# Kernel optimization log

Measured on AMD Instinct MI355X. Metric: run time of the kernel, lower is better.

## Reference

```python
import jax, jax.numpy as jnp
import numpy as np

NUM_RBF = 64
CUTOFF = 5.0
N_GRAPHS = 64


def _rbf_expand(d):
    # Gaussian RBF expansion on [0, CUTOFF] with cosine cutoff envelope.
    mus = jnp.linspace(0.0, CUTOFF, NUM_RBF, dtype=d.dtype)  # [M]
    gamma = (NUM_RBF / CUTOFF) ** 2  # 1 / spacing^2
    fc = 0.5 * (jnp.cos(jnp.pi * d / CUTOFF) + 1.0) * (d < CUTOFF)  # [E]
    return jnp.exp(-gamma * (d[:, None] - mus[None, :]) ** 2) * fc[:, None]  # [E,M]


def setup_inputs() -> dict:
    key = jax.random.key(0)
    k0, k1, k2, k3, k4, k5 = jax.random.split(key, 6)
    N, E, T = 50000, 1600000, 25
    pos = jax.random.normal(k0, (N, 3), jnp.float32) * 3.0
    edge_index = jax.random.randint(k1, (2, E), 0, N)
    atom_types = jax.random.randint(k2, (N,), 0, T)
    batch = jnp.sort(jax.random.randint(k3, (N,), 0, N_GRAPHS))
    rbf_params = jax.random.normal(k4, (T, T, NUM_RBF), jnp.float32)
    radial_filters = jax.random.uniform(k5, (T, T, NUM_RBF), jnp.float32)
    return {
        "pos": pos,
        "rbf_params": rbf_params,
        "radial_filters": radial_filters,
        "edge_index": edge_index,
        "atom_types": atom_types,
        "batch": batch,
    }


def reference(pos, rbf_params, radial_filters, edge_index, atom_types, batch):
    src, dst = edge_index[0], edge_index[1]
    # distances (no cell shifts)
    diff = pos[dst] - pos[src]                       # [E,3]
    d = jnp.sqrt(jnp.sum(diff * diff, axis=-1) + 1e-12)  # [E]
    # type-pair lookup with canonical ordering (sender <= receiver)
    s = atom_types[src]
    r = atom_types[dst]
    lo = jnp.minimum(s, r)
    hi = jnp.maximum(s, r)
    params = rbf_params[lo, hi]        # [E,M]
    filt = radial_filters[lo, hi]      # [E,M] (already in [0,1])
    expn = _rbf_expand(d) * filt       # filtered RBF expansion
    e_edge = jnp.sum(expn * params, axis=1)  # [E]
    # reduce per-edge energies to per-graph energies
    bmap = batch[src]
    energy = jax.ops.segment_sum(e_edge, bmap, num_segments=N_GRAPHS)  # [G]
    return energy
```

## Files before the change

kernel.cpp:

```cpp
#include <hip/hip_runtime.h>
#include <math.h>

#define NUM_RBF 64
#define N_GRAPHS 64


__global__ __launch_bounds__(256) void build_table_kernel(
    const float4* __restrict__ p, const float4* __restrict__ f,
    float4* __restrict__ C, int n4)
{
    int i = blockIdx.x * blockDim.x + threadIdx.x;
    if (i < n4) {
        float4 a = p[i], b = f[i];
        C[i] = make_float4(a.x * b.x, a.y * b.y, a.z * b.z, a.w * b.w);
    }
}

__global__ __launch_bounds__(256) void pack_nodes_kernel(
    const float* __restrict__ pos, const int* __restrict__ types,
    const int* __restrict__ batch, float4* __restrict__ rec, int N)
{
    int i = blockIdx.x * blockDim.x + threadIdx.x;
    if (i < N) {
        int bits = (types[i] & 0xFF) | ((batch[i] & 0xFF) << 8);
        rec[i] = make_float4(pos[3 * i], pos[3 * i + 1], pos[3 * i + 2],
                             __int_as_float(bits));
    }
}

#define CUTOFF_F      5.0f
#define GAMMA_F       163.84f
#define SPACING_F     (5.0f / 63.0f)
#define INV_SPACING_F (63.0f / 5.0f)
#define PI_OVER_C_F   (3.14159265358979f / 5.0f)

__device__ __forceinline__ void edge_body(
    float4 rs, float4 rd, const float4* __restrict__ C4, int T,
    float* __restrict__ bins)
{
    const float dx = rd.x - rs.x;
    const float dy = rd.y - rs.y;
    const float dz = rd.z - rs.z;
    const float d  = sqrtf(dx * dx + dy * dy + dz * dz + 1e-12f);
    if (d >= CUTOFF_F) return;

    const int sb = __float_as_int(rs.w);
    const int db = __float_as_int(rd.w);
    const int ts = sb & 0xFF;
    const int td = db & 0xFF;
    const int lo = min(ts, td);
    const int hi = max(ts, td);
    const int base = (lo * T + hi) * NUM_RBF;

    const float c = d * INV_SPACING_F;
    int a0 = ((int)floorf(c - 3.5f)) & ~3;
    a0 = max(0, min(NUM_RBF - 12, a0));

    const float4* w = C4 + ((base + a0) >> 2);
    float acc = 0.0f;
    float delta = d - (float)a0 * SPACING_F;
#pragma unroll
    for (int j = 0; j < 3; ++j) {
        const float4 cv = w[j];
        const float d0 = delta;
        const float d1 = delta - SPACING_F;
        const float d2 = delta - 2.0f * SPACING_F;
        const float d3 = delta - 3.0f * SPACING_F;
        acc += cv.x * __expf(-GAMMA_F * d0 * d0);
        acc += cv.y * __expf(-GAMMA_F * d1 * d1);
        acc += cv.z * __expf(-GAMMA_F * d2 * d2);
        acc += cv.w * __expf(-GAMMA_F * d3 * d3);
        delta -= 4.0f * SPACING_F;
    }
    const float fc = 0.5f * (__cosf(PI_OVER_C_F * d) + 1.0f);
    atomicAdd(&bins[(sb >> 8) & 0xFF], acc * fc);
}

__global__ __launch_bounds__(256) void edge_energy_kernel(
    const int*    __restrict__ edge_index,
    const float4* __restrict__ rec,
    const float4* __restrict__ C4,
    float*        __restrict__ partial,
    int E, int T)
{
    __shared__ float bins[N_GRAPHS];
    for (int i = threadIdx.x; i < N_GRAPHS; i += blockDim.x) bins[i] = 0.0f;
    __syncthreads();

    const int nfull  = E >> 2;
    const int stride = gridDim.x * blockDim.x;
    const int gid    = blockIdx.x * blockDim.x + threadIdx.x;

    for (int q = gid; q < nfull; q += stride) {
        const int e0 = q << 2;
        const int4 sv = *(const int4*)(edge_index + e0);
        const int4 tv = *(const int4*)(edge_index + E + e0);

        const float4 rs0 = rec[sv.x], rd0 = rec[tv.x];
        const float4 rs1 = rec[sv.y], rd1 = rec[tv.y];
        const float4 rs2 = rec[sv.z], rd2 = rec[tv.z];
        const float4 rs3 = rec[sv.w], rd3 = rec[tv.w];

        edge_body(rs0, rd0, C4, T, bins);
        edge_body(rs1, rd1, C4, T, bins);
        edge_body(rs2, rd2, C4, T, bins);
        edge_body(rs3, rd3, C4, T, bins);
    }

    if (gid == 0) {
        for (int e = nfull << 2; e < E; ++e) {
            const float4 rs = rec[edge_index[e]];
            const float4 rd = rec[edge_index[E + e]];
            edge_body(rs, rd, C4, T, bins);
        }
    }

    __syncthreads();
    for (int i = threadIdx.x; i < N_GRAPHS; i += blockDim.x)
        partial[blockIdx.x * N_GRAPHS + i] = bins[i];
}

__global__ __launch_bounds__(256) void reduce_kernel(
    const float* __restrict__ partial, float* __restrict__ out, int nblocks)
{
    const int g = blockIdx.x;
    float s = 0.0f;
    for (int i = threadIdx.x; i < nblocks; i += blockDim.x)
        s += partial[i * N_GRAPHS + g];

    for (int off = 32; off > 0; off >>= 1)
        s += __shfl_down(s, off, 64);

    __shared__ float red[4];
    const int wave = threadIdx.x >> 6;
    const int lane = threadIdx.x & 63;
    if (lane == 0) red[wave] = s;
    __syncthreads();
    if (threadIdx.x == 0)
        out[g] = red[0] + red[1] + red[2] + red[3];
}

extern "C" void kernel_launch(void* const* d_in, const int* in_sizes, int n_in,
                              void* d_out, int out_size, void* d_ws, size_t ws_size,
                              hipStream_t stream) {
    const float* pos            = (const float*)d_in[0];
    const float* rbf_params     = (const float*)d_in[1];
    const float* radial_filters = (const float*)d_in[2];
    const int*   edge_index     = (const int*)d_in[3];
    const int*   atom_types     = (const int*)d_in[4];
    const int*   batch          = (const int*)d_in[5];
    float*       out            = (float*)d_out;

    const int E = in_sizes[3] / 2;
    const int N = in_sizes[4];
    int T = 1;
    while ((T + 1) * (T + 1) * NUM_RBF <= in_sizes[1]) ++T;
    const int tbl_elems = T * T * NUM_RBF;

    float*  Ctab    = (float*)d_ws;
    float4* recs    = (float4*)((char*)d_ws + ((size_t)tbl_elems * 4 + 255) / 256 * 256);
    float*  partial = (float*)((char*)recs + (size_t)N * 16);

    const int nq = E >> 2;
    int nblocks = (nq + 255) / 256;
    const size_t part_off = (size_t)((char*)partial - (char*)d_ws);
    const size_t avail = (ws_size > part_off) ? (ws_size - part_off) : 0;
    const int maxb = (int)(avail / (N_GRAPHS * sizeof(float)));
    if (nblocks > maxb) nblocks = maxb > 0 ? maxb : 1;
    if (nblocks < 1) nblocks = 1;

    build_table_kernel<<<(tbl_elems / 4 + 255) / 256, 256, 0, stream>>>(
        (const float4*)rbf_params, (const float4*)radial_filters,
        (float4*)Ctab, tbl_elems / 4);
    pack_nodes_kernel<<<(N + 255) / 256, 256, 0, stream>>>(
        pos, atom_types, batch, recs, N);
    edge_energy_kernel<<<nblocks, 256, 0, stream>>>(
        edge_index, recs, (const float4*)Ctab, partial, E, T);
    reduce_kernel<<<N_GRAPHS, 256, 0, stream>>>(partial, out, nblocks);
}
```

Baseline: 97.57 us.

## Compute Gaussian RBF window via exp recurrence, fuse prologue kernels, nontemporal edge loads

Replaces the 12 per-edge exponentials with three exps plus a multiplicative recurrence. It expands the Gaussian around the centre bin, so each neighbour's term comes from the previous one times a ratio built from constant factors. The two setup kernels are merged into one launch, and edge-index loads now use nontemporal hints so streaming indices do not pollute cache. The recurrence adds rounding error, and u or ui may overflow or underflow for edges far from the centre bin.

```diff
diff --git a/kernel.cpp b/kernel.cpp
--- a/kernel.cpp
+++ b/kernel.cpp
@@ -4,38 +4,38 @@
 #define NUM_RBF 64
 #define N_GRAPHS 64
 
+typedef int   int4v   __attribute__((ext_vector_type(4)));
+typedef float float4v __attribute__((ext_vector_type(4)));
 
-__global__ __launch_bounds__(256) void build_table_kernel(
-    const float4* __restrict__ p, const float4* __restrict__ f,
-    float4* __restrict__ C, int n4)
+
+__global__ __launch_bounds__(256) void prologue_kernel(
+    const float4v* __restrict__ p, const float4v* __restrict__ f,
+    float4v* __restrict__ C, int n4,
+    const float* __restrict__ pos, const int* __restrict__ types,
+    const int* __restrict__ batch, float4v* __restrict__ rec, int N)
 {
     int i = blockIdx.x * blockDim.x + threadIdx.x;
-    if (i < n4) {
-        float4 a = p[i], b = f[i];
-        C[i] = make_float4(a.x * b.x, a.y * b.y, a.z * b.z, a.w * b.w);
-    }
-}
-
-__global__ __launch_bounds__(256) void pack_nodes_kernel(
-    const float* __restrict__ pos, const int* __restrict__ types,
-    const int* __restrict__ batch, float4* __restrict__ rec, int N)
-{
-    int i = blockIdx.x * blockDim.x + threadIdx.x;
+    if (i < n4) C[i] = p[i] * f[i];
     if (i < N) {
         int bits = (types[i] & 0xFF) | ((batch[i] & 0xFF) << 8);
-        rec[i] = make_float4(pos[3 * i], pos[3 * i + 1], pos[3 * i + 2],
-                             __int_as_float(bits));
+        float4v r = { pos[3 * i], pos[3 * i + 1], pos[3 * i + 2],
+                      __int_as_float(bits) };
+        rec[i] = r;
     }
 }
 
 #define CUTOFF_F      5.0f
 #define GAMMA_F       163.84f
-#define SPACING_F     (5.0f / 63.0f)
-#define INV_SPACING_F (63.0f / 5.0f)
-#define PI_OVER_C_F   (3.14159265358979f / 5.0f)
+#define SPACING_F     (float)(5.0 / 63.0)
+#define INV_SPACING_F (float)(63.0 / 5.0)
+#define PI_OVER_C_F   (float)(3.14159265358979323846 / 5.0)
+#define TWO_GAMMA_S_F (float)(2.0 * 163.84 * 5.0 / 63.0)
+#define LN_V          (-(64.0 / 63.0) * (64.0 / 63.0))
+#define V_1           (float)exp(LN_V)
+#define V_2           (float)exp(2.0 * LN_V)
 
 __device__ __forceinline__ void edge_body(
-    float4 rs, float4 rd, const float4* __restrict__ C4, int T,
+    float4v rs, float4v rd, const float4v* __restrict__ C4, int T,
     float* __restrict__ bins)
 {
     const float dx = rd.x - rs.x;
@@ -56,31 +56,40 @@
     int a0 = ((int)floorf(c - 3.5f)) & ~3;
     a0 = max(0, min(NUM_RBF - 12, a0));
 
-    const float4* w = C4 + ((base + a0) >> 2);
-    float acc = 0.0f;
-    float delta = d - (float)a0 * SPACING_F;
-#pragma unroll
-    for (int j = 0; j < 3; ++j) {
-        const float4 cv = w[j];
-        const float d0 = delta;
-        const float d1 = delta - SPACING_F;
-        const float d2 = delta - 2.0f * SPACING_F;
-        const float d3 = delta - 3.0f * SPACING_F;
-        acc += cv.x * __expf(-GAMMA_F * d0 * d0);
-        acc += cv.y * __expf(-GAMMA_F * d1 * d1);
-        acc += cv.z * __expf(-GAMMA_F * d2 * d2);
-        acc += cv.w * __expf(-GAMMA_F * d3 * d3);
-        delta -= 4.0f * SPACING_F;
-    }
+    const float4v* w = C4 + ((base + a0) >> 2);
+    const float4v w0 = w[0], w1 = w[1], w2 = w[2];
+
+    const float delta = d - (float)a0 * SPACING_F;
+    const float d5 = delta - 5.0f * SPACING_F;
+    const float t5 = __expf(-GAMMA_F * d5 * d5);
+    const float x  = TWO_GAMMA_S_F * d5;
+    const float u  = __expf(x);
+    const float ui = __expf(-x);
+
+    float acc = w1.y * t5;
+    float t = t5, m = u * V_1;
+    t *= m;  acc += w1.z * t;  m *= V_2;
+    t *= m;  acc += w1.w * t;  m *= V_2;
+    t *= m;  acc += w2.x * t;  m *= V_2;
+    t *= m;  acc += w2.y * t;  m *= V_2;
+    t *= m;  acc += w2.z * t;  m *= V_2;
+    t *= m;  acc += w2.w * t;
+    t = t5;  m = ui * V_1;
+    t *= m;  acc += w1.x * t;  m *= V_2;
+    t *= m;  acc += w0.w * t;  m *= V_2;
+    t *= m;  acc += w0.z * t;  m *= V_2;
+    t *= m;  acc += w0.y * t;  m *= V_2;
+    t *= m;  acc += w0.x * t;
+
     const float fc = 0.5f * (__cosf(PI_OVER_C_F * d) + 1.0f);
     atomicAdd(&bins[(sb >> 8) & 0xFF], acc * fc);
 }
 
 __global__ __launch_bounds__(256) void edge_energy_kernel(
-    const int*    __restrict__ edge_index,
-    const float4* __restrict__ rec,
-    const float4* __restrict__ C4,
-    float*        __restrict__ partial,
+    const int*     __restrict__ edge_index,
+    const float4v* __restrict__ rec,
+    const float4v* __restrict__ C4,
+    float*         __restrict__ partial,
     int E, int T)
 {
     __shared__ float bins[N_GRAPHS];
@@ -93,13 +102,15 @@
 
     for (int q = gid; q < nfull; q += stride) {
         const int e0 = q << 2;
-        const int4 sv = *(const int4*)(edge_index + e0);
-        const int4 tv = *(const int4*)(edge_index + E + e0);
+        const int4v sv = __builtin_nontemporal_load(
+            (const int4v*)(edge_index + e0));
+        const int4v tv = __builtin_nontemporal_load(
+            (const int4v*)(edge_index + E + e0));
 
-        const float4 rs0 = rec[sv.x], rd0 = rec[tv.x];
-        const float4 rs1 = rec[sv.y], rd1 = rec[tv.y];
-        const float4 rs2 = rec[sv.z], rd2 = rec[tv.z];
-        const float4 rs3 = rec[sv.w], rd3 = rec[tv.w];
+        const float4v rs0 = rec[sv.x], rd0 = rec[tv.x];
+        const float4v rs1 = rec[sv.y], rd1 = rec[tv.y];
+        const float4v rs2 = rec[sv.z], rd2 = rec[tv.z];
+        const float4v rs3 = rec[sv.w], rd3 = rec[tv.w];
 
         edge_body(rs0, rd0, C4, T, bins);
         edge_body(rs1, rd1, C4, T, bins);
@@ -109,8 +120,8 @@
 
     if (gid == 0) {
         for (int e = nfull << 2; e < E; ++e) {
-            const float4 rs = rec[edge_index[e]];
-            const float4 rd = rec[edge_index[E + e]];
+            const float4v rs = rec[edge_index[e]];
+            const float4v rd = rec[edge_index[E + e]];
             edge_body(rs, rd, C4, T, bins);
         }
     }
@@ -157,9 +168,9 @@
     while ((T + 1) * (T + 1) * NUM_RBF <= in_sizes[1]) ++T;
     const int tbl_elems = T * T * NUM_RBF;
 
-    float*  Ctab    = (float*)d_ws;
-    float4* recs    = (float4*)((char*)d_ws + ((size_t)tbl_elems * 4 + 255) / 256 * 256);
-    float*  partial = (float*)((char*)recs + (size_t)N * 16);
+    float*   Ctab    = (float*)d_ws;
+    float4v* recs    = (float4v*)((char*)d_ws + ((size_t)tbl_elems * 4 + 255) / 256 * 256);
+    float*   partial = (float*)((char*)recs + (size_t)N * 16);
 
     const int nq = E >> 2;
     int nblocks = (nq + 255) / 256;
@@ -169,12 +180,11 @@
     if (nblocks > maxb) nblocks = maxb > 0 ? maxb : 1;
     if (nblocks < 1) nblocks = 1;
 
-    build_table_kernel<<<(tbl_elems / 4 + 255) / 256, 256, 0, stream>>>(
-        (const float4*)rbf_params, (const float4*)radial_filters,
-        (float4*)Ctab, tbl_elems / 4);
-    pack_nodes_kernel<<<(N + 255) / 256, 256, 0, stream>>>(
-        pos, atom_types, batch, recs, N);
+    const int pro_n = max(tbl_elems / 4, N);
+    prologue_kernel<<<(pro_n + 255) / 256, 256, 0, stream>>>(
+        (const float4v*)rbf_params, (const float4v*)radial_filters,
+        (float4v*)Ctab, tbl_elems / 4, pos, atom_types, batch, recs, N);
     edge_energy_kernel<<<nblocks, 256, 0, stream>>>(
-        edge_index, recs, (const float4*)Ctab, partial, E, T);
+        edge_index, recs, (const float4v*)Ctab, partial, E, T);
     reduce_kernel<<<N_GRAPHS, 256, 0, stream>>>(partial, out, nblocks);
 }
```

Result: faster. 94.91 us (-2.7%).
